# Kernel tuning notes

Measured on AMD Instinct MI355X. Metric: run time of the kernel, lower is better.

## Reference

```python
import jax, jax.numpy as jnp
import numpy as np

N_NODES = 100000
N_EDGES = 1600000
IN_DIM = 29
OUT_DIM = 64
BN_EPS = 1e-5


def setup_inputs() -> dict:
    key = jax.random.key(0)
    k1, k2, k3, k4, k5, k6, k7, k8 = jax.random.split(key, 8)
    node = jax.random.normal(k1, (N_NODES, 3), dtype=jnp.float32)
    features = jax.random.normal(k2, (N_NODES, IN_DIM), dtype=jnp.float32)
    edges = jax.random.randint(k3, (N_EDGES, 2), 0, N_NODES, dtype=jnp.int64)
    # Linear(input_dim+3, output_dim, bias=False): weight [out, in+3]
    fan_in = IN_DIM + 3
    weight = jax.random.uniform(k4, (OUT_DIM, fan_in), dtype=jnp.float32,
                                minval=-1.0, maxval=1.0) / np.sqrt(fan_in)
    # BatchNorm1d(output_dim) in eval mode: affine params + running stats
    gamma = jax.random.normal(k5, (OUT_DIM,), dtype=jnp.float32) * 0.1 + 1.0
    beta = jax.random.normal(k6, (OUT_DIM,), dtype=jnp.float32) * 0.1
    running_mean = jax.random.normal(k7, (OUT_DIM,), dtype=jnp.float32) * 0.1
    running_var = jax.random.uniform(k8, (OUT_DIM,), dtype=jnp.float32,
                                     minval=0.5, maxval=1.5)
    return {"node": node, "features": features, "edges": edges,
            "weight": weight, "gamma": gamma, "beta": beta,
            "running_mean": running_mean, "running_var": running_var}


def reference(node, features, edges, weight, gamma, beta, running_mean, running_var):
    dst = edges[:, 0]  # pos_i index (pooling destination)
    src = edges[:, 1]  # pos_j / x_j index
    # gather + concat: msg [E, in+3]
    msg = jnp.concatenate([features[src], node[src] - node[dst]], axis=1)
    # Linear (no bias): [E, out]
    msg = jnp.einsum('ei,oi->eo', msg, weight)
    # BatchNorm1d (eval mode, running stats)
    inv_std = gamma / jnp.sqrt(running_var + BN_EPS)
    msg = (msg - running_mean) * inv_std + beta
    # scatter-max pooling over destination nodes (fixed N segments;
    # torch.unique + scatter_reduce(amax) == segment_max restricted to covered
    # nodes; empty segments filled with 0 matching the zeros init)
    pooled = jax.ops.segment_max(msg, dst, num_segments=N_NODES)
    return jnp.where(jnp.isneginf(pooled), 0.0, pooled)
```

## Files before the change

kernel.cpp:

```cpp
#include <hip/hip_runtime.h>
#include <hip/hip_fp16.h>

#define IN_DIM 29
#define XDIM 32
#define OUT_DIM 64
#define BN_EPS 1e-5f

#define BW      32
#define BW_LOG  5
#define PBLK    128
#define TBLK    2048
#define MAXBUCK 4096
#define SENT    0


__global__ __launch_bounds__(256) void fused_tc_kernel(
    const float* __restrict__ features, const float* __restrict__ node,
    const float* __restrict__ weight, const float* __restrict__ gamma,
    const float* __restrict__ rvar, unsigned short* __restrict__ yq,
    const int* __restrict__ edges, int* __restrict__ gHist,
    int n_nodes, int npw, int n_edges, int nbuck, int chunk_c, int cblk)
{
    if ((int)blockIdx.x < cblk) {
        __shared__ int h[MAXBUCK];
        for (int i = threadIdx.x; i < nbuck; i += 256) h[i] = 0;
        __syncthreads();
        const int e0 = blockIdx.x * chunk_c;
        const int e1 = min(e0 + chunk_c, n_edges);
        for (int e = e0 + threadIdx.x; e < e1; e += 256)
            atomicAdd(&h[edges[2*e] >> BW_LOG], 1);
        __syncthreads();
        for (int i = threadIdx.x; i < nbuck; i += 256)
            gHist[(size_t)i * cblk + blockIdx.x] = h[i];
    } else {
        const int lane = threadIdx.x & 63;
        const int wave = (((int)blockIdx.x - cblk) * 256 + (int)threadIdx.x) >> 6;
        int n0 = wave * npw;
        int n1 = n0 + npw; if (n1 > n_nodes) n1 = n_nodes;

        float w[XDIM];
        const float4* wp = (const float4*)(weight + lane * XDIM);
#pragma unroll
        for (int q = 0; q < 8; ++q) {
            float4 v = wp[q];
            w[4*q+0] = v.x; w[4*q+1] = v.y; w[4*q+2] = v.z; w[4*q+3] = v.w;
        }
        const float a = gamma[lane] * __frsqrt_rn(rvar[lane] + BN_EPS);

        for (int n = n0; n < n1; ++n) {
            const float* f = features + (size_t)n * IN_DIM;
            float acc = 0.0f;
#pragma unroll
            for (int i = 0; i < IN_DIM; ++i) acc = fmaf(f[i], w[i], acc);
            const float* nd = node + (size_t)n * 3;
#pragma unroll
            for (int j = 0; j < 3; ++j) acc = fmaf(nd[j], w[IN_DIM + j], acc);
            unsigned short hh = __half_as_ushort(__float2half(acc * a));
            unsigned short enc = (hh & 0x8000) ? (unsigned short)(~hh)
                                               : (unsigned short)(hh | 0x8000);
            yq[(size_t)n * OUT_DIM + lane] = enc;
        }
    }
}

__global__ __launch_bounds__(256) void scan_a_kernel(
    int* __restrict__ data, int n, int* __restrict__ aux)
{
    const int t = threadIdx.x;
    const int base = blockIdx.x * 1024 + t * 4;
    int v[4];
#pragma unroll
    for (int k = 0; k < 4; ++k) v[k] = (base + k < n) ? data[base + k] : 0;
    int tsum = v[0] + v[1] + v[2] + v[3];

    const int lane = t & 63, wv = t >> 6;
    int x = tsum;
#pragma unroll
    for (int off = 1; off < 64; off <<= 1) {
        int y = __shfl_up(x, off);
        if (lane >= off) x += y;
    }
    __shared__ int wsum[4];
    if (lane == 63) wsum[wv] = x;
    __syncthreads();
    int wexcl = 0;
    for (int i = 0; i < wv; ++i) wexcl += wsum[i];
    int run = wexcl + x - tsum;
#pragma unroll
    for (int k = 0; k < 4; ++k) {
        if (base + k < n) data[base + k] = run;
        run += v[k];
    }
    if (t == 255) aux[blockIdx.x] = run;
}

__global__ __launch_bounds__(256) void scan_b_kernel(int* __restrict__ aux, int nb) {
    const int t = threadIdx.x;
    const int lane = t & 63, wv = t >> 6;
    __shared__ int wsum[4];
    __shared__ int s_run;
    if (t == 0) s_run = 0;
    __syncthreads();
    for (int base = 0; base < nb; base += 256) {
        const int i = base + t;
        int v = (i < nb) ? aux[i] : 0;
        int x = v;
#pragma unroll
        for (int off = 1; off < 64; off <<= 1) {
            int y = __shfl_up(x, off);
            if (lane >= off) x += y;
        }
        if (lane == 63) wsum[wv] = x;
        __syncthreads();
        int wexcl = 0;
        for (int k = 0; k < wv; ++k) wexcl += wsum[k];
        const int run = s_run;
        if (i < nb) aux[i] = run + wexcl + x - v;
        __syncthreads();
        if (t == 255) s_run = run + wexcl + x;
        __syncthreads();
    }
}

__global__ __launch_bounds__(1024) void partition_kernel(
    const int* __restrict__ edges, const int* __restrict__ gOffs,
    const int* __restrict__ aux,
    int* __restrict__ keys, int n_edges, int nbuck, int chunk_c, int cblk)
{
    __shared__ int cur[MAXBUCK];
    const int R = cblk / PBLK;
    for (int i = threadIdx.x; i < nbuck; i += 1024) {
        const size_t idx = (size_t)i * cblk + R * blockIdx.x;
        cur[i] = gOffs[idx] + aux[idx >> 10];
    }
    __syncthreads();
    const int chunk_p = R * chunk_c;
    const int e0 = blockIdx.x * chunk_p;
    const int e1 = min(e0 + chunk_p, n_edges);
    for (int e = e0 + threadIdx.x; e < e1; e += 1024) {
        const int dst = edges[2*e], src = edges[2*e+1];
        const int b = dst >> BW_LOG;
        const int pos = atomicAdd(&cur[b], 1);
        keys[pos] = (dst & (BW - 1)) | (src << BW_LOG);
    }
}

__global__ __launch_bounds__(256) void pool_fused_kernel(
    const int* __restrict__ gOffs, const int* __restrict__ aux,
    const int* __restrict__ keys,
    const unsigned short* __restrict__ yq, const float* __restrict__ node,
    const float* __restrict__ weight, const float* __restrict__ gamma,
    const float* __restrict__ beta, const float* __restrict__ rmean,
    const float* __restrict__ rvar,
    float* __restrict__ out, int n_nodes, int n_edges, int nbuck, int cblk)
{
    __shared__ int acc[BW * OUT_DIM];
    const int tid = threadIdx.x;
    const int lane = tid & 63, wid = tid >> 6;
    const int b = blockIdx.x;

    {
        int4* p = (int4*)acc;
        for (int i = tid; i < BW * OUT_DIM / 4; i += 256)
            p[i] = make_int4(SENT, SENT, SENT, SENT);
    }
    __syncthreads();

    const size_t i0 = (size_t)b * cblk;
    const int beg = gOffs[i0] + aux[i0 >> 10];
    int end;
    if (b == nbuck - 1) end = n_edges;
    else {
        const size_t i1 = (size_t)(b + 1) * cblk;
        end = gOffs[i1] + aux[i1 >> 10];
    }

    const int cnt = end - beg;
    const int slice = (cnt + 3) >> 2;
    const int w_beg = beg + wid * slice;
    const int w_end = min(w_beg + slice, end);

    if (w_beg < w_end) {
        const int last = w_end - 1;
        int j = w_beg;
        int kv = keys[min(j + lane, last)];
        while (j < w_end) {
            const int jn = j + 64;
            int kv_n = 0;
            if (jn < w_end) kv_n = keys[min(jn + lane, last)];
            const int m = w_end - j < 64 ? w_end - j : 64;
            const int ng = (m + 7) >> 3;

            unsigned int va[8]; int da[8];
#pragma unroll
            for (int u = 0; u < 8; ++u) {
                const int uu = (u < m) ? u : (m - 1);
                const int key = __builtin_amdgcn_readlane(kv, uu);
                da[u] = key & (BW - 1);
                va[u] = yq[(size_t)((unsigned)key >> BW_LOG) * OUT_DIM + lane];
            }
            for (int g = 0; g < ng; ++g) {
                unsigned int vb[8]; int db[8];
                const bool more = (g + 1 < ng);
                if (more) {
#pragma unroll
                    for (int u = 0; u < 8; ++u) {
                        int uu = (g + 1) * 8 + u; uu = (uu < m) ? uu : (m - 1);
                        const int key = __builtin_amdgcn_readlane(kv, uu);
                        db[u] = key & (BW - 1);
                        vb[u] = yq[(size_t)((unsigned)key >> BW_LOG) * OUT_DIM + lane];
                    }
                }
#pragma unroll
                for (int u = 0; u < 8; ++u)
                    atomicMax(&acc[da[u] * OUT_DIM + lane], (int)va[u]);
                if (more) {
#pragma unroll
                    for (int u = 0; u < 8; ++u) { va[u] = vb[u]; da[u] = db[u]; }
                }
            }
            j = jn; kv = kv_n;
        }
    }
    __syncthreads();

    const float a  = gamma[lane] * __frsqrt_rn(rvar[lane] + BN_EPS);
    const float bp = beta[lane] - rmean[lane] * a;
    const float w29 = weight[lane * XDIM + 29] * a;
    const float w30 = weight[lane * XDIM + 30] * a;
    const float w31 = weight[lane * XDIM + 31] * a;

    for (int d = wid; d < BW; d += 4) {
        const int dg = b * BW + d;
        if (dg >= n_nodes) break;
        const int k = acc[d * OUT_DIM + lane];
        float rr;
        if (k == SENT) {
            rr = 0.0f;
        } else {
            const unsigned short enc = (unsigned short)k;
            const unsigned short h = (enc & 0x8000) ? (unsigned short)(enc ^ 0x8000)
                                                    : (unsigned short)(~enc);
            const float v = __half2float(__ushort_as_half(h));
            const float nx = node[(size_t)dg * 3 + 0];
            const float ny = node[(size_t)dg * 3 + 1];
            const float nz = node[(size_t)dg * 3 + 2];
            rr = v + (bp - (w29 * nx + w30 * ny + w31 * nz));
        }
        out[(size_t)dg * OUT_DIM + lane] = rr;
    }
}

__global__ void init_kernel(int4* __restrict__ out, int total4) {
    int t = blockIdx.x * blockDim.x + threadIdx.x;
    if (t < total4) out[t] = make_int4(INT_MIN, INT_MIN, INT_MIN, INT_MIN);
}

__global__ __launch_bounds__(256) void edge_atomic_kernel(
    const int* __restrict__ edges,
    const float* __restrict__ features, const float* __restrict__ node,
    const float* __restrict__ weight, const float* __restrict__ gamma,
    const float* __restrict__ beta, const float* __restrict__ rmean,
    const float* __restrict__ rvar,
    int* __restrict__ out, int n_edges, int epw)
{
    const int lane = threadIdx.x & 63;
    const int wave = (blockIdx.x * blockDim.x + threadIdx.x) >> 6;
    int e0 = wave * epw, e1 = e0 + epw;
    if (e1 > n_edges) e1 = n_edges;

    float w[XDIM];
    const float4* wp = (const float4*)(weight + lane * XDIM);
#pragma unroll
    for (int q = 0; q < 8; ++q) {
        float4 v = wp[q];
        w[4*q+0] = v.x; w[4*q+1] = v.y; w[4*q+2] = v.z; w[4*q+3] = v.w;
    }
    const float a = gamma[lane] * __frsqrt_rn(rvar[lane] + BN_EPS);
    const float bprime = beta[lane] - rmean[lane] * a;

    for (int e = e0; e < e1; ++e) {
        const int dst = edges[2*e+0], src = edges[2*e+1];
        float x[XDIM];
#pragma unroll
        for (int i = 0; i < IN_DIM; ++i) x[i] = features[(size_t)src * IN_DIM + i];
#pragma unroll
        for (int j = 0; j < 3; ++j)
            x[IN_DIM+j] = node[(size_t)src*3+j] - node[(size_t)dst*3+j];
        float acc = 0.0f;
#pragma unroll
        for (int i = 0; i < XDIM; ++i) acc = fmaf(x[i], w[i], acc);
        float msg = fmaf(acc, a, bprime);
        int bb = __float_as_int(msg);
        int key = (bb < 0) ? (bb ^ 0x7FFFFFFF) : bb;
        atomicMax(out + (size_t)dst * OUT_DIM + lane, key);
    }
}

__global__ void decode_kernel(int* __restrict__ out, int total) {
    int t = blockIdx.x * blockDim.x + threadIdx.x;
    if (t >= total) return;
    int k = out[t];
    float r;
    if (k == INT_MIN) r = 0.0f;
    else { int b = (k < 0) ? (k ^ 0x7FFFFFFF) : k; r = __int_as_float(b); }
    ((float*)out)[t] = r;
}

extern "C" void kernel_launch(void* const* d_in, const int* in_sizes, int n_in,
                              void* d_out, int out_size, void* d_ws, size_t ws_size,
                              hipStream_t stream) {
    const float* node     = (const float*)d_in[0];
    const float* features = (const float*)d_in[1];
    const int*   edges    = (const int*)d_in[2];
    const float* weight   = (const float*)d_in[3];
    const float* gamma    = (const float*)d_in[4];
    const float* beta     = (const float*)d_in[5];
    const float* rmean    = (const float*)d_in[6];
    const float* rvar     = (const float*)d_in[7];

    const int n_nodes = in_sizes[0] / 3;
    const int n_edges = in_sizes[2] / 2;

    const int nbuck = (n_nodes + BW - 1) >> BW_LOG;

    int cblk = 0; size_t o_yq=0, o_hist=0, o_aux=0, o_keys=0;
    for (int cand = 512; cand >= PBLK; cand >>= 1) {
        const size_t n_scan = (size_t)nbuck * cand;
        const size_t nb_scan = (n_scan + 1023) / 1024;
        size_t off = 0;
        auto alloc = [&](size_t bytes) { size_t r = off; off = (off + bytes + 15) & ~(size_t)15; return r; };
        o_yq   = alloc((size_t)n_nodes * OUT_DIM * sizeof(unsigned short));
        o_hist = alloc(n_scan * sizeof(int));
        o_aux  = alloc(nb_scan * sizeof(int));
        o_keys = alloc((size_t)n_edges * sizeof(int));
        if (off <= ws_size) { cblk = cand; break; }
    }

    if (cblk > 0 && nbuck <= MAXBUCK && n_nodes <= MAXBUCK * BW) {
        const int n_scan = nbuck * cblk;
        const int nb_scan = (n_scan + 1023) / 1024;
        const int chunk_c = (n_edges + cblk - 1) / cblk;
        const int npw = (n_nodes + TBLK * 4 - 1) / (TBLK * 4);

        char* base  = (char*)d_ws;
        unsigned short* yq = (unsigned short*)(base + o_yq);
        int* gHist  = (int*)(base + o_hist);
        int* aux    = (int*)(base + o_aux);
        int* keys   = (int*)(base + o_keys);

        fused_tc_kernel<<<cblk + TBLK, 256, 0, stream>>>(
            features, node, weight, gamma, rvar, yq,
            edges, gHist, n_nodes, npw, n_edges, nbuck, chunk_c, cblk);
        scan_a_kernel<<<nb_scan, 256, 0, stream>>>(gHist, n_scan, aux);
        scan_b_kernel<<<1, 256, 0, stream>>>(aux, nb_scan);
        partition_kernel<<<PBLK, 1024, 0, stream>>>(edges, gHist, aux, keys,
                                                    n_edges, nbuck, chunk_c, cblk);
        pool_fused_kernel<<<nbuck, 256, 0, stream>>>(
            gHist, aux, keys, yq, node, weight, gamma, beta, rmean, rvar,
            (float*)d_out, n_nodes, n_edges, nbuck, cblk);
    } else {
        int* out_i = (int*)d_out;
        const int total4 = out_size / 4;
        init_kernel<<<(total4 + 255) / 256, 256, 0, stream>>>((int4*)out_i, total4);
        const int n_waves = 8192;
        const int epw = (n_edges + n_waves - 1) / n_waves;
        edge_atomic_kernel<<<n_waves / 4, 256, 0, stream>>>(
            edges, features, node, weight, gamma, beta, rmean, rvar,
            out_i, n_edges, epw);
        decode_kernel<<<(out_size + 255) / 256, 256, 0, stream>>>(out_i, out_size);
    }
}
```

Baseline: 211.4 us.

## Transpose histogram layout and replace global scan with per-bucket column scan

The per-block histogram is now stored row-major by block (coalesced writes), and the full two-level prefix scan over nbuck*cblk entries is replaced by a column scan per bucket that only writes offsets at partition-block granularity, followed by a single-block scan over bucket totals. Partition and pooling kernels then read bucket base offsets directly. This cuts scan traffic and simplifies offset lookups. The cost is a serial loop over cblk per thread in the column scan and a single-block scan over roughly 3k buckets.

```diff
diff --git a/kernel.cpp b/kernel.cpp
--- a/kernel.cpp
+++ b/kernel.cpp
@@ -30,8 +30,8 @@
         for (int e = e0 + threadIdx.x; e < e1; e += 256)
             atomicAdd(&h[edges[2*e] >> BW_LOG], 1);
         __syncthreads();
-        for (int i = threadIdx.x; i < nbuck; i += 256)
-            gHist[(size_t)i * cblk + blockIdx.x] = h[i];
+        int* row = gHist + (size_t)blockIdx.x * nbuck;
+        for (int i = threadIdx.x; i < nbuck; i += 256) row[i] = h[i];
     } else {
         const int lane = threadIdx.x & 63;
         const int wave = (((int)blockIdx.x - cblk) * 256 + (int)threadIdx.x) >> 6;
@@ -63,35 +63,22 @@
     }
 }
 
-__global__ __launch_bounds__(256) void scan_a_kernel(
-    int* __restrict__ data, int n, int* __restrict__ aux)
-{
-    const int t = threadIdx.x;
-    const int base = blockIdx.x * 1024 + t * 4;
-    int v[4];
-#pragma unroll
-    for (int k = 0; k < 4; ++k) v[k] = (base + k < n) ? data[base + k] : 0;
-    int tsum = v[0] + v[1] + v[2] + v[3];
-
-    const int lane = t & 63, wv = t >> 6;
-    int x = tsum;
-#pragma unroll
-    for (int off = 1; off < 64; off <<= 1) {
-        int y = __shfl_up(x, off);
-        if (lane >= off) x += y;
-    }
-    __shared__ int wsum[4];
-    if (lane == 63) wsum[wv] = x;
-    __syncthreads();
-    int wexcl = 0;
-    for (int i = 0; i < wv; ++i) wexcl += wsum[i];
-    int run = wexcl + x - tsum;
-#pragma unroll
-    for (int k = 0; k < 4; ++k) {
-        if (base + k < n) data[base + k] = run;
-        run += v[k];
-    }
-    if (t == 255) aux[blockIdx.x] = run;
+__global__ __launch_bounds__(256) void colscan_kernel(
+    int* __restrict__ gHist, int* __restrict__ bTot,
+    int nbuck, int cblk, int R)
+{
+    const int i = blockIdx.x * 256 + threadIdx.x;
+    if (i >= nbuck) return;
+    int run = 0;
+    for (int j = 0; j < cblk; j += R) {
+        int t[4];
+#pragma unroll 4
+        for (int r = 0; r < R; ++r) t[r] = gHist[(size_t)(j + r) * nbuck + i];
+        gHist[(size_t)j * nbuck + i] = run;
+#pragma unroll 4
+        for (int r = 0; r < R; ++r) run += t[r];
+    }
+    bTot[i] = run;
 }
 
 __global__ __launch_bounds__(256) void scan_b_kernel(int* __restrict__ aux, int nb) {
@@ -123,16 +110,14 @@
 }
 
 __global__ __launch_bounds__(1024) void partition_kernel(
-    const int* __restrict__ edges, const int* __restrict__ gOffs,
-    const int* __restrict__ aux,
-    int* __restrict__ keys, int n_edges, int nbuck, int chunk_c, int cblk)
+    const int* __restrict__ edges, const int* __restrict__ gHist,
+    const int* __restrict__ bOffs,
+    int* __restrict__ keys, int n_edges, int nbuck, int chunk_c, int R)
 {
     __shared__ int cur[MAXBUCK];
-    const int R = cblk / PBLK;
-    for (int i = threadIdx.x; i < nbuck; i += 1024) {
-        const size_t idx = (size_t)i * cblk + R * blockIdx.x;
-        cur[i] = gOffs[idx] + aux[idx >> 10];
-    }
+    const int* prow = gHist + (size_t)(R * blockIdx.x) * nbuck;
+    for (int i = threadIdx.x; i < nbuck; i += 1024)
+        cur[i] = prow[i] + bOffs[i];
     __syncthreads();
     const int chunk_p = R * chunk_c;
     const int e0 = blockIdx.x * chunk_p;
@@ -146,13 +131,12 @@
 }
 
 __global__ __launch_bounds__(256) void pool_fused_kernel(
-    const int* __restrict__ gOffs, const int* __restrict__ aux,
-    const int* __restrict__ keys,
+    const int* __restrict__ bOffs, const int* __restrict__ keys,
     const unsigned short* __restrict__ yq, const float* __restrict__ node,
     const float* __restrict__ weight, const float* __restrict__ gamma,
     const float* __restrict__ beta, const float* __restrict__ rmean,
     const float* __restrict__ rvar,
-    float* __restrict__ out, int n_nodes, int n_edges, int nbuck, int cblk)
+    float* __restrict__ out, int n_nodes, int n_edges, int nbuck)
 {
     __shared__ int acc[BW * OUT_DIM];
     const int tid = threadIdx.x;
@@ -166,14 +150,8 @@
     }
     __syncthreads();
 
-    const size_t i0 = (size_t)b * cblk;
-    const int beg = gOffs[i0] + aux[i0 >> 10];
-    int end;
-    if (b == nbuck - 1) end = n_edges;
-    else {
-        const size_t i1 = (size_t)(b + 1) * cblk;
-        end = gOffs[i1] + aux[i1 >> 10];
-    }
+    const int beg = bOffs[b];
+    const int end = (b == nbuck - 1) ? n_edges : bOffs[b + 1];
 
     const int cnt = end - beg;
     const int slice = (cnt + 3) >> 2;
@@ -324,41 +302,39 @@
 
     const int nbuck = (n_nodes + BW - 1) >> BW_LOG;
 
-    int cblk = 0; size_t o_yq=0, o_hist=0, o_aux=0, o_keys=0;
+    int cblk = 0; size_t o_yq=0, o_hist=0, o_boffs=0, o_keys=0;
     for (int cand = 512; cand >= PBLK; cand >>= 1) {
-        const size_t n_scan = (size_t)nbuck * cand;
-        const size_t nb_scan = (n_scan + 1023) / 1024;
         size_t off = 0;
         auto alloc = [&](size_t bytes) { size_t r = off; off = (off + bytes + 15) & ~(size_t)15; return r; };
-        o_yq   = alloc((size_t)n_nodes * OUT_DIM * sizeof(unsigned short));
-        o_hist = alloc(n_scan * sizeof(int));
-        o_aux  = alloc(nb_scan * sizeof(int));
-        o_keys = alloc((size_t)n_edges * sizeof(int));
+        o_yq    = alloc((size_t)n_nodes * OUT_DIM * sizeof(unsigned short));
+        o_hist  = alloc((size_t)cand * nbuck * sizeof(int));
+        o_boffs = alloc((size_t)nbuck * sizeof(int));
+        o_keys  = alloc((size_t)n_edges * sizeof(int));
         if (off <= ws_size) { cblk = cand; break; }
     }
 
     if (cblk > 0 && nbuck <= MAXBUCK && n_nodes <= MAXBUCK * BW) {
-        const int n_scan = nbuck * cblk;
-        const int nb_scan = (n_scan + 1023) / 1024;
+        const int R = cblk / PBLK;
         const int chunk_c = (n_edges + cblk - 1) / cblk;
         const int npw = (n_nodes + TBLK * 4 - 1) / (TBLK * 4);
 
         char* base  = (char*)d_ws;
         unsigned short* yq = (unsigned short*)(base + o_yq);
         int* gHist  = (int*)(base + o_hist);
-        int* aux    = (int*)(base + o_aux);
+        int* bOffs  = (int*)(base + o_boffs);
         int* keys   = (int*)(base + o_keys);
 
         fused_tc_kernel<<<cblk + TBLK, 256, 0, stream>>>(
             features, node, weight, gamma, rvar, yq,
             edges, gHist, n_nodes, npw, n_edges, nbuck, chunk_c, cblk);
-        scan_a_kernel<<<nb_scan, 256, 0, stream>>>(gHist, n_scan, aux);
-        scan_b_kernel<<<1, 256, 0, stream>>>(aux, nb_scan);
-        partition_kernel<<<PBLK, 1024, 0, stream>>>(edges, gHist, aux, keys,
-                                                    n_edges, nbuck, chunk_c, cblk);
+        colscan_kernel<<<(nbuck + 255) / 256, 256, 0, stream>>>(
+            gHist, bOffs, nbuck, cblk, R);
+        scan_b_kernel<<<1, 256, 0, stream>>>(bOffs, nbuck);
+        partition_kernel<<<PBLK, 1024, 0, stream>>>(
+            edges, gHist, bOffs, keys, n_edges, nbuck, chunk_c, R);
         pool_fused_kernel<<<nbuck, 256, 0, stream>>>(
-            gHist, aux, keys, yq, node, weight, gamma, beta, rmean, rvar,
-            (float*)d_out, n_nodes, n_edges, nbuck, cblk);
+            bOffs, keys, yq, node, weight, gamma, beta, rmean, rvar,
+            (float*)d_out, n_nodes, n_edges, nbuck);
     } else {
         int* out_i = (int*)d_out;
         const int total4 = out_size / 4;
```

New measurement: 269.2 us. +27.3%, slower.
